# Performance work log

Hardware: AMD Instinct MI355X
Metric: run time of the kernel (lower is better)

Reference implementation:

```python
import jax, jax.numpy as jnp
import numpy as np

D_MODEL = 1024
N_HEADS = 16
D_K = D_MODEL // N_HEADS  # 64
B, T = 2, 2048


def setup_inputs() -> dict:
    key = jax.random.key(0)
    ks = jax.random.split(key, 6)
    s = 0.02
    x = jax.random.normal(ks[0], (B, T, D_MODEL), dtype=jnp.float32)
    # Stacked per-head projection weights, [H, C, d_k] (no bias, mini-gpt style)
    Wq = jax.random.normal(ks[1], (N_HEADS, D_MODEL, D_K), dtype=jnp.float32) * s
    Wk = jax.random.normal(ks[2], (N_HEADS, D_MODEL, D_K), dtype=jnp.float32) * s
    Wv = jax.random.normal(ks[3], (N_HEADS, D_MODEL, D_K), dtype=jnp.float32) * s
    # Output projection, torch nn.Linear(d_model, d_model): y = x @ Wo.T + bo
    Wo = jax.random.normal(ks[4], (D_MODEL, D_MODEL), dtype=jnp.float32) * s
    bo = jax.random.normal(ks[5], (D_MODEL,), dtype=jnp.float32) * s
    return {"x": x, "Wq": Wq, "Wk": Wk, "Wv": Wv, "Wo": Wo, "bo": bo}


def reference(x, Wq, Wk, Wv, Wo, bo):
    Bq, Tq, C = x.shape
    # Batched per-head projections (replaces the per-head Python loop)
    q = jnp.einsum('btc,hck->bhtk', x, Wq)  # [B,H,T,dk]
    k = jnp.einsum('btc,hck->bhtk', x, Wk)
    v = jnp.einsum('btc,hck->bhtk', x, Wv)
    scale = 1.0 / jnp.sqrt(jnp.asarray(D_K, dtype=x.dtype))
    scores = jnp.einsum('bhtk,bhsk->bhts', q, k) * scale  # [B,H,T,T]
    causal = jnp.tril(jnp.ones((Tq, Tq), dtype=bool))
    scores = jnp.where(causal, scores, jnp.asarray(-1e9, dtype=scores.dtype))
    attn = jax.nn.softmax(scores, axis=-1)
    out = jnp.einsum('bhts,bhsk->bhtk', attn, v)  # [B,H,T,dk]
    # concat heads -> [B,T,C]
    out = out.transpose(0, 2, 1, 3).reshape(Bq, Tq, C)
    return jnp.einsum('btc,dc->btd', out, Wo) + bo
```

## Files before the change

kernel.cpp:

```cpp
#include <hip/hip_runtime.h>
#include <hip/hip_bf16.h>


using short8 = __attribute__((ext_vector_type(8))) short;
using f32x4  = __attribute__((ext_vector_type(4))) float;
using fp16x2 = __attribute__((ext_vector_type(2))) __fp16;
using half4  = __attribute__((ext_vector_type(4))) _Float16;
using half8  = __attribute__((ext_vector_type(8))) _Float16;

#define SCALE_LOG2E 0.18033688011112042f

__device__ __forceinline__ unsigned short f2bf(float f) {
    union { float f; unsigned u; } v; v.f = f;
    unsigned r = v.u + 0x7fffu + ((v.u >> 16) & 1u);
    return (unsigned short)(r >> 16);
}

__device__ __forceinline__ void gld16(const unsigned short* gp, unsigned short* lp) {
    __builtin_amdgcn_global_load_lds(
        (const __attribute__((address_space(1))) void*)(gp),
        (__attribute__((address_space(3))) void*)(unsigned int)(unsigned long long)(lp),
        16, 0, 0);
}

__global__ void cvt_bf16(const float* __restrict__ in,
                         unsigned short* __restrict__ out, int n4) {
    int i = blockIdx.x * blockDim.x + threadIdx.x;
    if (i >= n4) return;
    float4 v = ((const float4*)in)[i];
    ushort4 o;
    o.x = f2bf(v.x); o.y = f2bf(v.y); o.z = f2bf(v.z); o.w = f2bf(v.w);
    ((ushort4*)out)[i] = o;
}

__global__ void transpose_w(const float* __restrict__ Wq,
                            const float* __restrict__ Wk,
                            const float* __restrict__ Wv,
                            unsigned short* __restrict__ out) {
    __shared__ float tile[64][65];
    int b = blockIdx.x;
    int cchunk = b & 15;
    int h = (b >> 4) & 15;
    int s = b >> 8;
    const float* W = (s == 0) ? Wq : ((s == 1) ? Wk : Wv);
    float sc = (s == 0) ? SCALE_LOG2E : 1.0f;
    const float* src = W + (h * 1024 + cchunk * 64) * 64;
    int t = threadIdx.x;
    #pragma unroll
    for (int it = 0; it < 4; ++it) {
        int idx = (it * 256 + t) * 4;
        int cc = idx >> 6, kk = idx & 63;
        float4 v = *(const float4*)(src + idx);
        tile[cc][kk + 0] = v.x; tile[cc][kk + 1] = v.y;
        tile[cc][kk + 2] = v.z; tile[cc][kk + 3] = v.w;
    }
    __syncthreads();
    unsigned short* dst = out + (size_t)((s * 16 + h) * 64) * 1024 + cchunk * 64;
    #pragma unroll
    for (int it = 0; it < 16; ++it) {
        int idx = it * 256 + t;
        int kk = idx >> 6, cc = idx & 63;
        dst[kk * 1024 + cc] = f2bf(tile[cc][kk] * sc);
    }
}

#define GEMM_CORE(A_, B_, m0_, n0_)                                          \
    __shared__ unsigned short Als[128 * 32];                                 \
    __shared__ unsigned short Bls[128 * 32];                                 \
    int wave = threadIdx.x >> 6;                                             \
    int lane = threadIdx.x & 63;                                             \
    int col  = lane & 15;                                                    \
    int quad = lane >> 4;                                                    \
    int m_off = (wave & 1) * 64;                                             \
    int n_off = (wave >> 1) * 64;                                            \
    int ldr = lane >> 2;                                                     \
    int ldc = (lane & 3) * 8;                                                \
    f32x4 acc[4][4] = {};                                                    \
    for (int k0 = 0; k0 < 1024; k0 += 32) {                                  \
        __syncthreads();                                                     \
        _Pragma("unroll")                                                    \
        for (int j = 0; j < 2; ++j) {                                        \
            int row = wave * 32 + j * 16;                                    \
            gld16(A_ + (size_t)(m0_ + row + ldr) * 1024 + k0 + ldc,          \
                  Als + row * 32);                                           \
            gld16(B_ + (size_t)(n0_ + row + ldr) * 1024 + k0 + ldc,          \
                  Bls + row * 32);                                           \
        }                                                                    \
        __syncthreads();                                                     \
        short8 af[4], bf[4];                                                 \
        _Pragma("unroll")                                                    \
        for (int i = 0; i < 4; ++i) {                                        \
            af[i] = *(const short8*)(Als + (m_off + i * 16 + col) * 32 + quad * 8); \
            bf[i] = *(const short8*)(Bls + (n_off + i * 16 + col) * 32 + quad * 8); \
        }                                                                    \
        _Pragma("unroll")                                                    \
        for (int mb = 0; mb < 4; ++mb)                                       \
            _Pragma("unroll")                                                \
            for (int nb = 0; nb < 4; ++nb)                                   \
                acc[mb][nb] = __builtin_amdgcn_mfma_f32_16x16x32_bf16(       \
                    af[mb], bf[nb], acc[mb][nb], 0, 0, 0);                   \
    }

__global__ __launch_bounds__(256) void qkv_gemm(
        const unsigned short* __restrict__ xb,
        const unsigned short* __restrict__ Wt,
        unsigned short* __restrict__ qB,
        unsigned short* __restrict__ kfrag,
        _Float16* __restrict__ vfrag) {
    int m0 = blockIdx.x * 128;
    int n0 = blockIdx.y * 128;
    GEMM_CORE(xb, Wt, m0, n0)
    int sel = blockIdx.y >> 3;
    #pragma unroll
    for (int nb = 0; nb < 4; ++nb) {
        int n = n0 + n_off + nb * 16 + col;
        int d10 = n & 1023;
        int h_ = d10 >> 6, d = d10 & 63;
        if (sel == 0) {
            #pragma unroll
            for (int mb = 0; mb < 4; ++mb)
                #pragma unroll
                for (int r = 0; r < 4; ++r) {
                    int m = m0 + m_off + mb * 16 + quad * 4 + r;
                    int b_ = m >> 11, t_ = m & 2047;
                    qB[((size_t)(b_ * 16 + h_) * 2048 + t_) * 64 + d] =
                        f2bf(acc[mb][nb][r]);
                }
        } else if (sel == 1) {
            int hK = d >> 5, quadk = (d >> 3) & 3, j = d & 7;
            #pragma unroll
            for (int mb = 0; mb < 4; ++mb)
                #pragma unroll
                for (int r = 0; r < 4; ++r) {
                    int m = m0 + m_off + mb * 16 + quad * 4 + r;
                    int b_ = m >> 11, t_ = m & 2047;
                    int bh = b_ * 16 + h_;
                    kfrag[((((size_t)bh * 128 + (t_ >> 4)) * 2 + hK) * 64 +
                           quadk * 16 + (t_ & 15)) * 8 + j] = f2bf(acc[mb][nb][r]);
                }
        } else {
            int nbv = d >> 4, colv = d & 15;
            #pragma unroll
            for (int mb = 0; mb < 4; ++mb)
                #pragma unroll
                for (int r = 0; r < 4; ++r) {
                    int m = m0 + m_off + mb * 16 + quad * 4 + r;
                    int b_ = m >> 11, t_ = m & 2047;
                    int bh = b_ * 16 + h_;
                    vfrag[((((size_t)bh * 64 + (t_ >> 5)) * 4 + nbv) * 64 +
                           ((t_ >> 2) & 3) * 16 + colv) * 8 +
                          ((t_ >> 4) & 1) * 4 + (t_ & 3)] = (_Float16)acc[mb][nb][r];
                }
        }
    }
}

__global__ __launch_bounds__(256) void oproj(
        const unsigned short* __restrict__ A,
        const unsigned short* __restrict__ Bw,
        const float* __restrict__ bo,
        float* __restrict__ y) {
    int m0 = blockIdx.x * 128;
    int n0 = blockIdx.y * 128;
    GEMM_CORE(A, Bw, m0, n0)
    #pragma unroll
    for (int nb = 0; nb < 4; ++nb) {
        int n = n0 + n_off + nb * 16 + col;
        float bias = bo[n];
        #pragma unroll
        for (int mb = 0; mb < 4; ++mb)
            #pragma unroll
            for (int r = 0; r < 4; ++r) {
                int m = m0 + m_off + mb * 16 + quad * 4 + r;
                y[(size_t)m * 1024 + n] = acc[mb][nb][r] + bias;
            }
    }
}

__global__ __launch_bounds__(256, 4) void attn(
        const unsigned short* __restrict__ qB,
        const unsigned short* __restrict__ kfrag,
        const _Float16* __restrict__ vfrag,
        unsigned short* __restrict__ aout) {
    __shared__ float O_comb[2][64][33];
    __shared__ float L_comb[2][2][2][16];
    int wave = threadIdx.x >> 6;
    int lane = threadIdx.x & 63;
    int col  = lane & 15;
    int quad = lane >> 4;
    int sl     = wave >> 1;
    int parity = wave & 1;
    int bh   = blockIdx.x & 31;
    int pairidx = 31 - (blockIdx.x >> 5);
    int strip = pairidx * 2 + sl;
    int q0 = strip * 32;
    const unsigned short* q = qB + (size_t)bh * 2048 * 64;
    const unsigned short* kf_base = kfrag + (size_t)bh * 128 * 2 * 512;
    const _Float16*       vf_base = vfrag + (size_t)bh * 64 * 4 * 512;

    short8 qf[2][2];
    #pragma unroll
    for (int qb = 0; qb < 2; ++qb)
        #pragma unroll
        for (int h = 0; h < 2; ++h)
            qf[qb][h] = *(const short8*)(q + (size_t)(q0 + qb * 16 + col) * 64 + h * 32 + quad * 8);

    f32x4 o[2][4] = {};
    float l[2] = {0.f, 0.f};

    int n_iter = (q0 + 95) >> 6;
    for (int it = parity; it < n_iter; it += 2) {
        int kv0 = it * 64;
        bool diag = (kv0 + 63 > q0);
        #pragma unroll
        for (int kv32 = 0; kv32 < 2; ++kv32) {
            half8 vv[4];
            #pragma unroll
            for (int nb = 0; nb < 4; ++nb)
                vv[nb] = *(const half8*)(vf_base +
                    (((size_t)((kv0 >> 5) + kv32) * 4 + nb) * 64 + lane) * 8);
            #pragma unroll
            for (int par = 0; par < 2; ++par) {
                int kvb = kv32 * 2 + par;
                int kvbase = kv0 + kvb * 16;
                int K16 = (kv0 >> 4) + kvb;
                short8 kf0 = *(const short8*)(kf_base + (((size_t)K16 * 2 + 0) * 64 + lane) * 8);
                short8 kf1 = *(const short8*)(kf_base + (((size_t)K16 * 2 + 1) * 64 + lane) * 8);
                f32x4 st[2] = {};
                #pragma unroll
                for (int qb = 0; qb < 2; ++qb) {
                    st[qb] = __builtin_amdgcn_mfma_f32_16x16x32_bf16(kf0, qf[qb][0], st[qb], 0, 0, 0);
                    st[qb] = __builtin_amdgcn_mfma_f32_16x16x32_bf16(kf1, qf[qb][1], st[qb], 0, 0, 0);
                }
                #pragma unroll
                for (int qb = 0; qb < 2; ++qb) {
                    float p0 = __builtin_amdgcn_exp2f(st[qb][0]);
                    float p1 = __builtin_amdgcn_exp2f(st[qb][1]);
                    float p2 = __builtin_amdgcn_exp2f(st[qb][2]);
                    float p3 = __builtin_amdgcn_exp2f(st[qb][3]);
                    if (diag) {
                        int qg  = q0 + qb * 16 + col;
                        int kvg = kvbase + quad * 4;
                        p0 = (kvg + 0 > qg) ? 0.f : p0;
                        p1 = (kvg + 1 > qg) ? 0.f : p1;
                        p2 = (kvg + 2 > qg) ? 0.f : p2;
                        p3 = (kvg + 3 > qg) ? 0.f : p3;
                    }
                    l[qb] += (p0 + p1) + (p2 + p3);
                    union { fp16x2 h2[2]; half4 h4; } cvt;
                    cvt.h2[0] = __builtin_amdgcn_cvt_pkrtz(p0, p1);
                    cvt.h2[1] = __builtin_amdgcn_cvt_pkrtz(p2, p3);
                    half4 pf = cvt.h4;
                    #pragma unroll
                    for (int nb = 0; nb < 4; ++nb) {
                        half4 vf = (par == 0)
                            ? __builtin_shufflevector(vv[nb], vv[nb], 0, 1, 2, 3)
                            : __builtin_shufflevector(vv[nb], vv[nb], 4, 5, 6, 7);
                        o[qb][nb] = __builtin_amdgcn_mfma_f32_16x16x16f16(pf, vf, o[qb][nb], 0, 0, 0);
                    }
                }
            }
        }
    }
    #pragma unroll
    for (int qb = 0; qb < 2; ++qb) {
        float lr = l[qb];
        lr += __shfl_xor(lr, 16);
        lr += __shfl_xor(lr, 32);
        l[qb] = lr;
    }
    if (quad == 0) {
        L_comb[sl][parity][0][col] = l[0];
        L_comb[sl][parity][1][col] = l[1];
    }
    if (parity == 1) {
        #pragma unroll
        for (int qb = 0; qb < 2; ++qb)
            #pragma unroll
            for (int nb = 0; nb < 4; ++nb)
                #pragma unroll
                for (int r = 0; r < 4; ++r)
                    O_comb[sl][lane][qb * 16 + nb * 4 + r] = o[qb][nb][r];
    }
    __syncthreads();
    if (parity == 0) {
        int b_ = bh >> 4, h_ = bh & 15;
        #pragma unroll
        for (int qb = 0; qb < 2; ++qb)
            #pragma unroll
            for (int r = 0; r < 4; ++r) {
                int qi = quad * 4 + r;
                float inv_l = 1.0f / (L_comb[sl][0][qb][qi] + L_comb[sl][1][qb][qi]);
                int t_ = q0 + qb * 16 + qi;
                #pragma unroll
                for (int nb = 0; nb < 4; ++nb) {
                    float ov = o[qb][nb][r] + O_comb[sl][lane][qb * 16 + nb * 4 + r];
                    aout[(size_t)(b_ * 2048 + t_) * 1024 + h_ * 64 + nb * 16 + col] =
                        f2bf(ov * inv_l);
                }
            }
    }
}

extern "C" void kernel_launch(void* const* d_in, const int* in_sizes, int n_in,
                              void* d_out, int out_size, void* d_ws, size_t ws_size,
                              hipStream_t stream) {
    const float* x  = (const float*)d_in[0];
    const float* Wq = (const float*)d_in[1];
    const float* Wk = (const float*)d_in[2];
    const float* Wv = (const float*)d_in[3];
    const float* Wo = (const float*)d_in[4];
    const float* bo = (const float*)d_in[5];
    float* y = (float*)d_out;

    unsigned short* xb    = (unsigned short*)d_ws;
    unsigned short* Wt    = xb    + 4194304;
    unsigned short* Wob   = Wt    + 3145728;
    unsigned short* qBb   = Wob   + 1048576;
    unsigned short* kfr   = qBb   + 4194304;
    unsigned short* vfr   = kfr   + 4194304;
    unsigned short* aout  = vfr   + 4194304;

    cvt_bf16<<<4096, 256, 0, stream>>>(x,  xb,  1048576);
    cvt_bf16<<<1024, 256, 0, stream>>>(Wo, Wob, 262144);
    transpose_w<<<768, 256, 0, stream>>>(Wq, Wk, Wv, Wt);
    qkv_gemm<<<dim3(32, 24), 256, 0, stream>>>(xb, Wt, qBb, kfr, (_Float16*)vfr);
    attn<<<1024, 256, 0, stream>>>(qBb, kfr, (const _Float16*)vfr, aout);
    oproj<<<dim3(32, 8), 256, 0, stream>>>(aout, Wob, bo, y);
}
```

Baseline: 191.5 us.

## Double-buffer K/V register loads in attention, widen GEMM K-tile with swizzled LDS

The attention loop now prefetches the next half-tile of K and V fragments into a second register buffer while computing on the current one, so global load latency overlaps with MFMA work. To make room for the extra registers, the occupancy hint is lowered from 4 to 3 blocks per CU. The shared GEMM core doubles its K step to 64 and uses an XOR-swizzled LDS layout to avoid bank conflicts, which halves the number of barriers. The V-fragment epilogue now writes four halves per vector store instead of scalar stores. The risks are higher register pressure and lower occupancy in attention, and more LDS per GEMM block.

```diff
diff --git a/kernel.cpp b/kernel.cpp
--- a/kernel.cpp
+++ b/kernel.cpp
@@ -65,40 +65,45 @@
 }
 
 #define GEMM_CORE(A_, B_, m0_, n0_)                                          \
-    __shared__ unsigned short Als[128 * 32];                                 \
-    __shared__ unsigned short Bls[128 * 32];                                 \
+    __shared__ unsigned short Als[128 * 64];                                 \
+    __shared__ unsigned short Bls[128 * 64];                                 \
     int wave = threadIdx.x >> 6;                                             \
     int lane = threadIdx.x & 63;                                             \
     int col  = lane & 15;                                                    \
     int quad = lane >> 4;                                                    \
     int m_off = (wave & 1) * 64;                                             \
     int n_off = (wave >> 1) * 64;                                            \
-    int ldr = lane >> 2;                                                     \
-    int ldc = (lane & 3) * 8;                                                \
+    int ldr = lane >> 3;                                                     \
+    int ldc = ((lane & 7) ^ ldr) * 8;                                        \
     f32x4 acc[4][4] = {};                                                    \
-    for (int k0 = 0; k0 < 1024; k0 += 32) {                                  \
+    for (int k0 = 0; k0 < 1024; k0 += 64) {                                  \
         __syncthreads();                                                     \
         _Pragma("unroll")                                                    \
-        for (int j = 0; j < 2; ++j) {                                        \
-            int row = wave * 32 + j * 16;                                    \
+        for (int j = 0; j < 4; ++j) {                                        \
+            int row = wave * 32 + j * 8;                                     \
             gld16(A_ + (size_t)(m0_ + row + ldr) * 1024 + k0 + ldc,          \
-                  Als + row * 32);                                           \
+                  Als + row * 64);                                           \
             gld16(B_ + (size_t)(n0_ + row + ldr) * 1024 + k0 + ldc,          \
-                  Bls + row * 32);                                           \
+                  Bls + row * 64);                                           \
         }                                                                    \
         __syncthreads();                                                     \
-        short8 af[4], bf[4];                                                 \
         _Pragma("unroll")                                                    \
-        for (int i = 0; i < 4; ++i) {                                        \
-            af[i] = *(const short8*)(Als + (m_off + i * 16 + col) * 32 + quad * 8); \
-            bf[i] = *(const short8*)(Bls + (n_off + i * 16 + col) * 32 + quad * 8); \
+        for (int kh = 0; kh < 2; ++kh) {                                     \
+            short8 af[4], bf[4];                                             \
+            _Pragma("unroll")                                                \
+            for (int i = 0; i < 4; ++i) {                                    \
+                int lc = kh * 4 + quad;                                      \
+                int sw = (lc ^ (col & 7)) * 8;                               \
+                af[i] = *(const short8*)(Als + (m_off + i * 16 + col) * 64 + sw); \
+                bf[i] = *(const short8*)(Bls + (n_off + i * 16 + col) * 64 + sw); \
+            }                                                                \
+            _Pragma("unroll")                                                \
+            for (int mb = 0; mb < 4; ++mb)                                   \
+                _Pragma("unroll")                                            \
+                for (int nb = 0; nb < 4; ++nb)                               \
+                    acc[mb][nb] = __builtin_amdgcn_mfma_f32_16x16x32_bf16(   \
+                        af[mb], bf[nb], acc[mb][nb], 0, 0, 0);               \
         }                                                                    \
-        _Pragma("unroll")                                                    \
-        for (int mb = 0; mb < 4; ++mb)                                       \
-            _Pragma("unroll")                                                \
-            for (int nb = 0; nb < 4; ++nb)                                   \
-                acc[mb][nb] = __builtin_amdgcn_mfma_f32_16x16x32_bf16(       \
-                    af[mb], bf[nb], acc[mb][nb], 0, 0, 0);                   \
     }
 
 __global__ __launch_bounds__(256) void qkv_gemm(
@@ -141,16 +146,16 @@
         } else {
             int nbv = d >> 4, colv = d & 15;
             #pragma unroll
-            for (int mb = 0; mb < 4; ++mb)
-                #pragma unroll
-                for (int r = 0; r < 4; ++r) {
-                    int m = m0 + m_off + mb * 16 + quad * 4 + r;
-                    int b_ = m >> 11, t_ = m & 2047;
-                    int bh = b_ * 16 + h_;
-                    vfrag[((((size_t)bh * 64 + (t_ >> 5)) * 4 + nbv) * 64 +
-                           ((t_ >> 2) & 3) * 16 + colv) * 8 +
-                          ((t_ >> 4) & 1) * 4 + (t_ & 3)] = (_Float16)acc[mb][nb][r];
-                }
+            for (int mb = 0; mb < 4; ++mb) {
+                int m = m0 + m_off + mb * 16 + quad * 4;
+                int b_ = m >> 11, t_ = m & 2047;
+                int bh = b_ * 16 + h_;
+                half4 hv;
+                hv[0] = (_Float16)acc[mb][nb][0]; hv[1] = (_Float16)acc[mb][nb][1];
+                hv[2] = (_Float16)acc[mb][nb][2]; hv[3] = (_Float16)acc[mb][nb][3];
+                *(half4*)(vfrag + ((((size_t)bh * 64 + (t_ >> 5)) * 4 + nbv) * 64 +
+                          ((t_ >> 2) & 3) * 16 + colv) * 8 + ((t_ >> 4) & 1) * 4) = hv;
+            }
         }
     }
 }
@@ -177,7 +182,7 @@
     }
 }
 
-__global__ __launch_bounds__(256, 4) void attn(
+__global__ __launch_bounds__(256, 3) void attn(
         const unsigned short* __restrict__ qB,
         const unsigned short* __restrict__ kfrag,
         const _Float16* __restrict__ vfrag,
@@ -208,60 +213,74 @@
     f32x4 o[2][4] = {};
     float l[2] = {0.f, 0.f};
 
-    int n_iter = (q0 + 95) >> 6;
-    for (int it = parity; it < n_iter; it += 2) {
+    struct KV { short8 kf[2][2]; half8 vv[4]; };
+    KV bufA, bufB;
+
+    auto load_half = [&](int it, int kv32, KV& b) {
+        int K16 = it * 4 + kv32 * 2;
+        #pragma unroll
+        for (int p = 0; p < 2; ++p)
+            #pragma unroll
+            for (int h = 0; h < 2; ++h)
+                b.kf[p][h] = *(const short8*)(kf_base +
+                    (((size_t)(K16 + p) * 2 + h) * 64 + lane) * 8);
+        #pragma unroll
+        for (int nb = 0; nb < 4; ++nb)
+            b.vv[nb] = *(const half8*)(vf_base +
+                (((size_t)(it * 2 + kv32) * 4 + nb) * 64 + lane) * 8);
+    };
+
+    auto compute_half = [&](int it, int kv32, KV& b) {
         int kv0 = it * 64;
         bool diag = (kv0 + 63 > q0);
         #pragma unroll
-        for (int kv32 = 0; kv32 < 2; ++kv32) {
-            half8 vv[4];
-            #pragma unroll
-            for (int nb = 0; nb < 4; ++nb)
-                vv[nb] = *(const half8*)(vf_base +
-                    (((size_t)((kv0 >> 5) + kv32) * 4 + nb) * 64 + lane) * 8);
-            #pragma unroll
-            for (int par = 0; par < 2; ++par) {
-                int kvb = kv32 * 2 + par;
-                int kvbase = kv0 + kvb * 16;
-                int K16 = (kv0 >> 4) + kvb;
-                short8 kf0 = *(const short8*)(kf_base + (((size_t)K16 * 2 + 0) * 64 + lane) * 8);
-                short8 kf1 = *(const short8*)(kf_base + (((size_t)K16 * 2 + 1) * 64 + lane) * 8);
-                f32x4 st[2] = {};
-                #pragma unroll
-                for (int qb = 0; qb < 2; ++qb) {
-                    st[qb] = __builtin_amdgcn_mfma_f32_16x16x32_bf16(kf0, qf[qb][0], st[qb], 0, 0, 0);
-                    st[qb] = __builtin_amdgcn_mfma_f32_16x16x32_bf16(kf1, qf[qb][1], st[qb], 0, 0, 0);
-                }
-                #pragma unroll
-                for (int qb = 0; qb < 2; ++qb) {
-                    float p0 = __builtin_amdgcn_exp2f(st[qb][0]);
-                    float p1 = __builtin_amdgcn_exp2f(st[qb][1]);
-                    float p2 = __builtin_amdgcn_exp2f(st[qb][2]);
-                    float p3 = __builtin_amdgcn_exp2f(st[qb][3]);
-                    if (diag) {
-                        int qg  = q0 + qb * 16 + col;
-                        int kvg = kvbase + quad * 4;
-                        p0 = (kvg + 0 > qg) ? 0.f : p0;
-                        p1 = (kvg + 1 > qg) ? 0.f : p1;
-                        p2 = (kvg + 2 > qg) ? 0.f : p2;
-                        p3 = (kvg + 3 > qg) ? 0.f : p3;
-                    }
-                    l[qb] += (p0 + p1) + (p2 + p3);
-                    union { fp16x2 h2[2]; half4 h4; } cvt;
-                    cvt.h2[0] = __builtin_amdgcn_cvt_pkrtz(p0, p1);
-                    cvt.h2[1] = __builtin_amdgcn_cvt_pkrtz(p2, p3);
-                    half4 pf = cvt.h4;
-                    #pragma unroll
-                    for (int nb = 0; nb < 4; ++nb) {
-                        half4 vf = (par == 0)
-                            ? __builtin_shufflevector(vv[nb], vv[nb], 0, 1, 2, 3)
-                            : __builtin_shufflevector(vv[nb], vv[nb], 4, 5, 6, 7);
-                        o[qb][nb] = __builtin_amdgcn_mfma_f32_16x16x16f16(pf, vf, o[qb][nb], 0, 0, 0);
-                    }
+        for (int par = 0; par < 2; ++par) {
+            int kvbase = kv0 + kv32 * 32 + par * 16;
+            f32x4 st[2] = {};
+            #pragma unroll
+            for (int qb = 0; qb < 2; ++qb) {
+                st[qb] = __builtin_amdgcn_mfma_f32_16x16x32_bf16(b.kf[par][0], qf[qb][0], st[qb], 0, 0, 0);
+                st[qb] = __builtin_amdgcn_mfma_f32_16x16x32_bf16(b.kf[par][1], qf[qb][1], st[qb], 0, 0, 0);
+            }
+            #pragma unroll
+            for (int qb = 0; qb < 2; ++qb) {
+                float p0 = __builtin_amdgcn_exp2f(st[qb][0]);
+                float p1 = __builtin_amdgcn_exp2f(st[qb][1]);
+                float p2 = __builtin_amdgcn_exp2f(st[qb][2]);
+                float p3 = __builtin_amdgcn_exp2f(st[qb][3]);
+                if (diag) {
+                    int qg  = q0 + qb * 16 + col;
+                    int kvg = kvbase + quad * 4;
+                    p0 = (kvg + 0 > qg) ? 0.f : p0;
+                    p1 = (kvg + 1 > qg) ? 0.f : p1;
+                    p2 = (kvg + 2 > qg) ? 0.f : p2;
+                    p3 = (kvg + 3 > qg) ? 0.f : p3;
+                }
+                l[qb] += (p0 + p1) + (p2 + p3);
+                union { fp16x2 h2[2]; half4 h4; } cvt;
+                cvt.h2[0] = __builtin_amdgcn_cvt_pkrtz(p0, p1);
+                cvt.h2[1] = __builtin_amdgcn_cvt_pkrtz(p2, p3);
+                half4 pf = cvt.h4;
+                #pragma unroll
+                for (int nb = 0; nb < 4; ++nb) {
+                    half4 vf = (par == 0)
+                        ? __builtin_shufflevector(b.vv[nb], b.vv[nb], 0, 1, 2, 3)
+                        : __builtin_shufflevector(b.vv[nb], b.vv[nb], 4, 5, 6, 7);
+                    o[qb][nb] = __builtin_amdgcn_mfma_f32_16x16x16f16(pf, vf, o[qb][nb], 0, 0, 0);
                 }
             }
         }
-    }
+    };
+
+    int n_iter = (q0 + 95) >> 6;
+    if (parity < n_iter) load_half(parity, 0, bufA);
+    for (int it = parity; it < n_iter; it += 2) {
+        load_half(it, 1, bufB);
+        compute_half(it, 0, bufA);
+        if (it + 2 < n_iter) load_half(it + 2, 0, bufA);
+        compute_half(it, 1, bufB);
+    }
+
     #pragma unroll
     for (int qb = 0; qb < 2; ++qb) {
         float lr = l[qb];
```

New measurement: 182.0 us. -5.0%, faster.
